# Optimization experiments

Hardware: AMD Instinct MI355X
Metric: run time of the kernel (lower is better)

Reference implementation:

```python
import jax, jax.numpy as jnp
import numpy as np

B, T, C_IN, H, W = 4, 128, 8, 32, 32
K = 9
HID = 64
N_BLOCKS = 2


def _conv(x, w, b):
    # x: [N, Cin, H, W], w: [Cout, Cin, 3, 3]
    y = jax.lax.conv_general_dilated(x, w, (1, 1), 'SAME',
                                     dimension_numbers=('NCHW', 'OIHW', 'NCHW'))
    return y + b[None, :, None, None]


def _refiner(x, w_in, b_in, w1s, b1s, w2s, b2s, w_out, b_out):
    # conv_in -> N_BLOCKS residual blocks -> conv_out (assumed LatentResidualRefiner structure)
    h = jax.nn.silu(_conv(x, w_in, b_in))
    for i in range(w1s.shape[0]):
        h = h + _conv(jax.nn.silu(_conv(h, w1s[i], b1s[i])), w2s[i], b2s[i])
    return _conv(h, w_out, b_out)


def setup_inputs() -> dict:
    key = jax.random.key(0)
    ks = jax.random.split(key, 8)
    latents = jax.random.normal(ks[0], (B, T, C_IN, H, W), dtype=jnp.float32)
    # distinct sorted anchor indices per batch row (duplicates would create zero-length gaps)
    idx = jax.vmap(lambda k: jnp.sort(jax.random.choice(k, T, (K,), replace=False)))(
        jax.random.split(ks[1], B)).astype(jnp.int32)
    in_ch = 3 * C_IN + 1   # z_base, z0, z1, t_chan (gap_cond=False)
    out_ch = C_IN + 1      # residual + uncertainty channel
    s = jnp.float32(0.05)
    w_in = jax.random.normal(ks[2], (HID, in_ch, 3, 3), jnp.float32) * s
    b_in = jnp.zeros((HID,), jnp.float32)
    w1s = jax.random.normal(ks[3], (N_BLOCKS, HID, HID, 3, 3), jnp.float32) * s
    b1s = jnp.zeros((N_BLOCKS, HID), jnp.float32)
    w2s = jax.random.normal(ks[4], (N_BLOCKS, HID, HID, 3, 3), jnp.float32) * s
    b2s = jnp.zeros((N_BLOCKS, HID), jnp.float32)
    w_out = jax.random.normal(ks[5], (out_ch, HID, 3, 3), jnp.float32) * s
    b_out = jnp.zeros((out_ch,), jnp.float32)
    return dict(latents=latents, idx=idx, w_in=w_in, b_in=b_in, w1s=w1s, b1s=b1s,
                w2s=w2s, b2s=b2s, w_out=w_out, b_out=b_out)


def reference(latents, idx, w_in, b_in, w1s, b1s, w2s, b2s, w_out, b_out):
    # Fully vectorized version of LatentLerpResidualInterpolator.interpolate:
    # every timestep finds its bracketing anchors (t0, t1); alpha clamping makes
    # anchors and out-of-range edges reduce exactly to the anchor latents
    # (scale = alpha*(1-alpha) = 0), matching the per-segment torch loop.
    Bb, Tt, C, Hh, Ww = latents.shape
    Kk = idx.shape[1]
    dt = latents.dtype
    idx_s = jnp.sort(idx, axis=1)                                   # [B,K]
    t = jnp.arange(Tt)
    seg = jax.vmap(lambda ib: jnp.searchsorted(ib, t, side='right'))(idx_s) - 1
    seg = jnp.clip(seg, 0, Kk - 2)                                  # [B,T]
    t0 = jnp.take_along_axis(idx_s, seg, axis=1)                    # [B,T]
    t1 = jnp.take_along_axis(idx_s, seg + 1, axis=1)                # [B,T]
    alpha_raw = (t[None, :] - t0).astype(dt) / jnp.maximum(t1 - t0, 1).astype(dt)
    alpha = jnp.clip(alpha_raw, 0.0, 1.0)                           # [B,T]
    gather = jax.vmap(lambda lat, i: lat[i])
    z0 = gather(latents, t0)                                        # [B,T,C,H,W]
    z1 = gather(latents, t1)
    a = alpha[:, :, None, None, None]
    z_base = (1.0 - a) * z0 + a * z1
    t_chan = jnp.broadcast_to(a, (Bb, Tt, 1, Hh, Ww)).astype(dt)
    res_in = jnp.concatenate([z_base, z0, z1, t_chan], axis=2)
    res_in = res_in.reshape(Bb * Tt, 3 * C + 1, Hh, Ww)
    out = _refiner(res_in, w_in, b_in, w1s, b1s, w2s, b2s, w_out, b_out)
    out = out.reshape(Bb, Tt, C + 1, Hh, Ww)
    res = out[:, :, :C]
    unc = jax.nn.sigmoid(out[:, :, C])                              # [B,T,H,W]
    z_hat = z_base + (a * (1.0 - a)) * res                          # [B,T,C,H,W]
    interior = (alpha_raw > 0.0) & (alpha_raw < 1.0)                # strict gap interior
    conf = jnp.where(interior[:, :, None, None],
                     jnp.clip(1.0 - unc, 0.0, 1.0), jnp.asarray(1.0, dt))
    return z_hat, conf
```

## Files before the change

kernel.cpp:

```cpp
#include <hip/hip_runtime.h>
#include <hip/hip_bf16.h>

#define DEVFN __device__ __forceinline__

typedef __attribute__((ext_vector_type(8))) short bf16x8;
typedef __attribute__((ext_vector_type(4))) float f32x4;

constexpr int T = 128, C = 8, K = 9;
constexpr int HW = 1024;
constexpr int BT = 512;
constexpr size_t Z_SIZE = (size_t)BT * C * HW;

constexpr int ROW_B = 34 * 128;
constexpr int BUF_B = 34 * ROW_B;

constexpr int WP_IN = 0;
constexpr int WP_W1_0 = 18432;
constexpr int WP_W2_0 = 55296;
constexpr int WP_W1_1 = 92160;
constexpr int WP_W2_1 = 129024;
constexpr int WP_OUT = 165888;
constexpr int WP_TOT = 175104;

DEVFN ushort f2bs(float x) {
  __hip_bfloat16 h = __float2bfloat16(x);
  ushort u;
  __builtin_memcpy(&u, &h, 2);
  return u;
}
DEVFN float bs2f(ushort u) {
  __hip_bfloat16 h;
  __builtin_memcpy(&h, &u, 2);
  return __bfloat162float(h);
}

DEVFN void interp_params(const int* __restrict__ idx, int b, int t,
                         int& t0, int& t1, float& ar, float& a) {
  const int* ib = idx + b * K;
  int cnt = 0;
#pragma unroll
  for (int k = 0; k < K; ++k) cnt += (ib[k] <= t) ? 1 : 0;
  int seg = min(max(cnt - 1, 0), K - 2);
  t0 = ib[seg];
  t1 = ib[seg + 1];
  ar = (float)(t - t0) / (float)max(t1 - t0, 1);
  a = fminf(fmaxf(ar, 0.f), 1.f);
}

__global__ __launch_bounds__(256) void pack_weights(
    const float* __restrict__ w_in, const float* __restrict__ w1s,
    const float* __restrict__ w2s, const float* __restrict__ w_out,
    __hip_bfloat16* __restrict__ wp) {
  int e = blockIdx.x * 256 + threadIdx.x;
  if (e >= WP_TOT) return;
  float v;
  if (e < WP_W1_0) {
    int tap = e / 2048;
    int r2 = e % 2048;
    int mt = r2 / 512;
    int lane = (r2 / 8) & 63;
    int el = e & 7;
    int oc = mt * 16 + (lane & 15);
    int ic = (lane >> 4) * 8 + el;
    v = (ic < 25) ? w_in[((size_t)oc * 25 + ic) * 9 + tap] : 0.f;
  } else if (e < WP_OUT) {
    int r = e - WP_W1_0;
    int layer = r / 36864;
    int r2 = r % 36864;
    int tap = r2 / 4096;
    int c = (r2 / 2048) & 1;
    int mt = (r2 / 512) & 3;
    int lane = (r2 / 8) & 63;
    int el = r2 & 7;
    int oc = mt * 16 + (lane & 15);
    int ic = c * 32 + (lane >> 4) * 8 + el;
    const float* src = (layer & 1) ? w2s : w1s;
    int blk = layer >> 1;
    v = src[(((size_t)blk * 64 + oc) * 64 + ic) * 9 + tap];
  } else {
    int r2 = e - WP_OUT;
    int tap = r2 / 1024;
    int c = (r2 / 512) & 1;
    int lane = (r2 / 8) & 63;
    int el = r2 & 7;
    int oc = lane & 15;
    int ic = c * 32 + (lane >> 4) * 8 + el;
    v = (oc < 9) ? w_out[((size_t)oc * 64 + ic) * 9 + tap] : 0.f;
  }
  wp[e] = __float2bfloat16(v);
}

template <int CK, int MT>
DEVFN void conv_compute(const char* sBuf, const __hip_bfloat16* __restrict__ wpf,
                        const int (&base)[3][2], int lane,
                        f32x4 (&acc)[MT][4]) {
#pragma unroll
  for (int c = 0; c < CK; ++c) {
#pragma unroll
    for (int d = 0; d < 3; ++d) {
      bf16x8 bv[4][2];
#pragma unroll
      for (int j = 0; j < 4; ++j)
#pragma unroll
        for (int xh = 0; xh < 2; ++xh)
          bv[j][xh] = *(const bf16x8*)(sBuf + base[d][c] + xh * 2048 + j * ROW_B);
#pragma unroll
      for (int mt = 0; mt < MT; ++mt) {
#pragma unroll
        for (int dyi = 0; dyi < 3; ++dyi) {
          const int tap = dyi * 3 + d;
          bf16x8 av =
              *(const bf16x8*)(wpf + (((tap * CK + c) * MT + mt) * 64 + lane) * 8);
#pragma unroll
          for (int oy = 0; oy < 2; ++oy)
#pragma unroll
            for (int xh = 0; xh < 2; ++xh)
              acc[mt][oy * 2 + xh] = __builtin_amdgcn_mfma_f32_16x16x32_bf16(
                  av, bv[oy + dyi][xh], acc[mt][oy * 2 + xh], 0, 0, 0);
        }
      }
    }
  }
}

DEVFN int wr_off(int nt) { return (nt & 1) * 2048 + ((nt >> 1) + 1) * ROW_B; }

DEVFN void layer_write_silu(char* sBuf, const int (&wbase)[4],
                            const float* __restrict__ bias, int g,
                            const f32x4 (&acc)[4][4]) {
#pragma unroll
  for (int mt = 0; mt < 4; ++mt) {
    const float4 bv = *(const float4*)(bias + mt * 16 + g * 4);
#pragma unroll
    for (int nt = 0; nt < 4; ++nt) {
      ushort4 s;
      float x0 = acc[mt][nt][0] + bv.x;
      float x1 = acc[mt][nt][1] + bv.y;
      float x2 = acc[mt][nt][2] + bv.z;
      float x3 = acc[mt][nt][3] + bv.w;
      s.x = f2bs(x0 / (1.f + expf(-x0)));
      s.y = f2bs(x1 / (1.f + expf(-x1)));
      s.z = f2bs(x2 / (1.f + expf(-x2)));
      s.w = f2bs(x3 / (1.f + expf(-x3)));
      *(ushort4*)(sBuf + wbase[mt] + wr_off(nt)) = s;
    }
  }
}

DEVFN void layer_write_bias(char* sBuf, const int (&wbase)[4],
                            const float* __restrict__ bias, int g,
                            const f32x4 (&acc)[4][4]) {
#pragma unroll
  for (int mt = 0; mt < 4; ++mt) {
    const float4 bv = *(const float4*)(bias + mt * 16 + g * 4);
#pragma unroll
    for (int nt = 0; nt < 4; ++nt) {
      ushort4 s;
      s.x = f2bs(acc[mt][nt][0] + bv.x);
      s.y = f2bs(acc[mt][nt][1] + bv.y);
      s.z = f2bs(acc[mt][nt][2] + bv.z);
      s.w = f2bs(acc[mt][nt][3] + bv.w);
      *(ushort4*)(sBuf + wbase[mt] + wr_off(nt)) = s;
    }
  }
}

__global__ __launch_bounds__(1024) void mega_kernel(
    const float* __restrict__ latents, const int* __restrict__ idx,
    const __hip_bfloat16* __restrict__ wpk, const float* __restrict__ b_in,
    const float* __restrict__ b1s, const float* __restrict__ b2s,
    const float* __restrict__ b_out, float* __restrict__ dout) {
  __shared__ __align__(16) char sBuf[BUF_B];

  const int img = blockIdx.x;
  const int tid = threadIdx.x;
  const int lane = tid & 63;
  const int wv = tid >> 6;
  const int g = lane >> 4;
  const int ln = lane & 15;
  const int r0 = wv * 2;
  const int b = img >> 7, t = img & 127;

  int t0, t1;
  float ar, a;
  interp_params(idx, b, t, t0, t1, ar, a);
  const float* z0p = latents + ((size_t)b * T + t0) * C * HW;
  const float* z1p = latents + ((size_t)b * T + t1) * C * HW;

  if (tid < 132) {
    int sy, sx;
    if (tid < 34) { sy = 0; sx = tid; }
    else if (tid < 68) { sy = 33; sx = tid - 34; }
    else { int r = tid - 68; sy = 1 + (r >> 1); sx = (r & 1) * 33; }
    int4* p4 = (int4*)(sBuf + sy * ROW_B + sx * 128);
#pragma unroll
    for (int q = 0; q < 8; ++q) p4[q] = int4{0, 0, 0, 0};
  }
  {
    const ushort ab = f2bs(a);
    const int si = tid;
    const int y = si >> 5, x = si & 31;
    const int sy = y + 1, sx = x + 1;
    const int key = (sx & 7) << 4;
    char* rowp = sBuf + sy * ROW_B + sx * 128;
    float v0[8], v1[8];
#pragma unroll
    for (int c2 = 0; c2 < 8; ++c2) {
      v0[c2] = z0p[c2 * HW + si];
      v1[c2] = z1p[c2 * HW + si];
    }
    ushort u[8];
    int4 q;
#pragma unroll
    for (int c2 = 0; c2 < 8; ++c2) u[c2] = f2bs((1.f - a) * v0[c2] + a * v1[c2]);
    q.x = (int)u[0] | ((int)u[1] << 16); q.y = (int)u[2] | ((int)u[3] << 16);
    q.z = (int)u[4] | ((int)u[5] << 16); q.w = (int)u[6] | ((int)u[7] << 16);
    *(int4*)(rowp + (0 ^ key)) = q;
#pragma unroll
    for (int c2 = 0; c2 < 8; ++c2) u[c2] = f2bs(v0[c2]);
    q.x = (int)u[0] | ((int)u[1] << 16); q.y = (int)u[2] | ((int)u[3] << 16);
    q.z = (int)u[4] | ((int)u[5] << 16); q.w = (int)u[6] | ((int)u[7] << 16);
    *(int4*)(rowp + (16 ^ key)) = q;
#pragma unroll
    for (int c2 = 0; c2 < 8; ++c2) u[c2] = f2bs(v1[c2]);
    q.x = (int)u[0] | ((int)u[1] << 16); q.y = (int)u[2] | ((int)u[3] << 16);
    q.z = (int)u[4] | ((int)u[5] << 16); q.w = (int)u[6] | ((int)u[7] << 16);
    *(int4*)(rowp + (32 ^ key)) = q;
    q.x = (int)ab; q.y = 0; q.z = 0; q.w = 0;
    *(int4*)(rowp + (48 ^ key)) = q;
  }
  __syncthreads();

  int base[3][2];
#pragma unroll
  for (int d = 0; d < 3; ++d)
#pragma unroll
    for (int c = 0; c < 2; ++c)
      base[d][c] = r0 * ROW_B +
                   (((ln + d) * 128 + c * 64 + g * 16) ^ (((ln + d) & 7) << 4));
  const int wkey = ((ln + 1) & 7) << 4;
  int wbase[4];
#pragma unroll
  for (int mt = 0; mt < 4; ++mt)
    wbase[mt] = r0 * ROW_B + (ln + 1) * 128 + ((mt * 32 + g * 8) ^ wkey);

  {
    f32x4 acc[4][4];
#pragma unroll
    for (int mt = 0; mt < 4; ++mt)
#pragma unroll
      for (int nt = 0; nt < 4; ++nt) acc[mt][nt] = (f32x4)0.f;
    conv_compute<1, 4>(sBuf, wpk + WP_IN, base, lane, acc);
    __syncthreads();
    layer_write_silu(sBuf, wbase, b_in, g, acc);
    __syncthreads();
  }

#pragma unroll 1
  for (int blk = 0; blk < 2; ++blk) {
    const __hip_bfloat16* wp1 = wpk + (blk ? WP_W1_1 : WP_W1_0);
    const __hip_bfloat16* wp2 = wpk + (blk ? WP_W2_1 : WP_W2_0);
    ushort4 hs[4][4];
    {
      f32x4 acc[4][4];
#pragma unroll
      for (int mt = 0; mt < 4; ++mt)
#pragma unroll
        for (int nt = 0; nt < 4; ++nt) acc[mt][nt] = (f32x4)0.f;
      conv_compute<2, 4>(sBuf, wp1, base, lane, acc);
#pragma unroll
      for (int mt = 0; mt < 4; ++mt)
#pragma unroll
        for (int nt = 0; nt < 4; ++nt)
          hs[mt][nt] = *(const ushort4*)(sBuf + wbase[mt] + wr_off(nt));
      __syncthreads();
      layer_write_silu(sBuf, wbase, b1s + blk * 64, g, acc);
      __syncthreads();
    }
    {
      f32x4 acc[4][4];
#pragma unroll
      for (int mt = 0; mt < 4; ++mt)
#pragma unroll
        for (int nt = 0; nt < 4; ++nt) {
          f32x4 h4;
          h4[0] = bs2f(hs[mt][nt].x);
          h4[1] = bs2f(hs[mt][nt].y);
          h4[2] = bs2f(hs[mt][nt].z);
          h4[3] = bs2f(hs[mt][nt].w);
          acc[mt][nt] = h4;
        }
      conv_compute<2, 4>(sBuf, wp2, base, lane, acc);
      __syncthreads();
      layer_write_bias(sBuf, wbase, b2s + blk * 64, g, acc);
      __syncthreads();
    }
  }

  {
    f32x4 acc[1][4];
#pragma unroll
    for (int nt = 0; nt < 4; ++nt) acc[0][nt] = (f32x4)0.f;
    conv_compute<2, 1>(sBuf, wpk + WP_OUT, base, lane, acc);
    __syncthreads();
#pragma unroll
    for (int nt = 0; nt < 4; ++nt) {
      ushort4 s;
      s.x = f2bs(acc[0][nt][0]);
      s.y = f2bs(acc[0][nt][1]);
      s.z = f2bs(acc[0][nt][2]);
      s.w = f2bs(acc[0][nt][3]);
      *(ushort4*)(sBuf + wbase[0] + wr_off(nt)) = s;
    }
    __syncthreads();
  }

  const bool interior = (ar > 0.f) && (ar < 1.f);
  const float aa = a * (1.f - a);
  {
    const int px = tid;
    const int y = px >> 5, x = px & 31;
    const int sy = y + 1, sx = x + 1;
    const int key = (sx & 7) << 4;
    const char* rp = sBuf + sy * ROW_B + sx * 128;
    bf16x8 r8 = *(const bf16x8*)(rp + (0 ^ key));
    int r9i = *(const int*)(rp + (16 ^ key));
    float res[9];
#pragma unroll
    for (int e = 0; e < 8; ++e) res[e] = bs2f((ushort)r8[e]);
    res[8] = bs2f((ushort)(r9i & 0xffff));
#pragma unroll
    for (int c2 = 0; c2 < 8; ++c2) {
      float v0 = z0p[c2 * HW + px], v1 = z1p[c2 * HW + px];
      float zb = (1.f - a) * v0 + a * v1;
      dout[((size_t)img * C + c2) * HW + px] = zb + aa * (res[c2] + b_out[c2]);
    }
    float unc = 1.f / (1.f + expf(-(res[8] + b_out[8])));
    float conf = interior ? fminf(fmaxf(1.f - unc, 0.f), 1.f) : 1.f;
    dout[Z_SIZE + (size_t)img * HW + px] = conf;
  }
}

extern "C" void kernel_launch(void* const* d_in, const int* in_sizes, int n_in,
                              void* d_out, int out_size, void* d_ws,
                              size_t ws_size, hipStream_t stream) {
  const float* latents = (const float*)d_in[0];
  const int* idx = (const int*)d_in[1];
  const float* w_in = (const float*)d_in[2];
  const float* b_in = (const float*)d_in[3];
  const float* w1s = (const float*)d_in[4];
  const float* b1s = (const float*)d_in[5];
  const float* w2s = (const float*)d_in[6];
  const float* b2s = (const float*)d_in[7];
  const float* w_out = (const float*)d_in[8];
  const float* b_out = (const float*)d_in[9];
  float* dout = (float*)d_out;

  __hip_bfloat16* wpk = (__hip_bfloat16*)d_ws;

  pack_weights<<<(WP_TOT + 255) / 256, 256, 0, stream>>>(w_in, w1s, w2s, w_out,
                                                         wpk);
  mega_kernel<<<BT, 1024, 0, stream>>>(latents, idx, wpk, b_in, b1s, b2s, b_out,
                                       dout);
}
```

Before: 283.4 us.

## Split fused per-image refiner into per-layer row-tiled conv kernels via global memory

Replaces the single 1024-thread-per-image megakernel with six launches, one per conv layer. Each launch uses 256-thread blocks that each handle an 8-row strip, and bf16 activations round-trip through workspace buffers in global memory, with the residual add done in the epilogue. The aim is smaller LDS footprint per block and a 4x larger grid for better occupancy and latency hiding. In exchange it adds global-memory traffic for intermediate activations (about 64 MB per layer), recomputes halo rows, and pays extra launch overhead.

```diff
diff --git a/kernel.cpp b/kernel.cpp
--- a/kernel.cpp
+++ b/kernel.cpp
@@ -11,8 +11,10 @@
 constexpr int BT = 512;
 constexpr size_t Z_SIZE = (size_t)BT * C * HW;
 
-constexpr int ROW_B = 34 * 128;
-constexpr int BUF_B = 34 * ROW_B;
+constexpr int SROW64 = 34 * 128;
+constexpr int TILE64 = 10 * SROW64;
+constexpr int SROW32 = 34 * 64;
+constexpr int TILE32 = 10 * SROW32;
 
 constexpr int WP_IN = 0;
 constexpr int WP_W1_0 = 18432;
@@ -90,10 +92,12 @@
   wp[e] = __float2bfloat16(v);
 }
 
-template <int CK, int MT>
+template <int CK, int MT, int SITE_B>
 DEVFN void conv_compute(const char* sBuf, const __hip_bfloat16* __restrict__ wpf,
-                        const int (&base)[3][2], int lane,
+                        const int (&base)[3][CK], int lane,
                         f32x4 (&acc)[MT][4]) {
+  constexpr int ROW = 34 * SITE_B;
+  constexpr int XH = 16 * SITE_B;
 #pragma unroll
   for (int c = 0; c < CK; ++c) {
 #pragma unroll
@@ -103,7 +107,7 @@
       for (int j = 0; j < 4; ++j)
 #pragma unroll
         for (int xh = 0; xh < 2; ++xh)
-          bv[j][xh] = *(const bf16x8*)(sBuf + base[d][c] + xh * 2048 + j * ROW_B);
+          bv[j][xh] = *(const bf16x8*)(sBuf + base[d][c] + xh * XH + j * ROW);
 #pragma unroll
       for (int mt = 0; mt < MT; ++mt) {
 #pragma unroll
@@ -123,62 +127,97 @@
   }
 }
 
-DEVFN int wr_off(int nt) { return (nt & 1) * 2048 + ((nt >> 1) + 1) * ROW_B; }
-
-DEVFN void layer_write_silu(char* sBuf, const int (&wbase)[4],
-                            const float* __restrict__ bias, int g,
-                            const f32x4 (&acc)[4][4]) {
+template <bool SILU, bool RESID>
+__global__ __launch_bounds__(256) void conv64_t(
+    const __hip_bfloat16* __restrict__ in,
+    const __hip_bfloat16* __restrict__ wpf,
+    const float* __restrict__ bias,
+    __hip_bfloat16* __restrict__ out) {
+  __shared__ __align__(16) char sBuf[TILE64];
+
+  const int img = blockIdx.x;
+  const int R0 = blockIdx.y * 8;
+  const int tid = threadIdx.x;
+  const int lane = tid & 63, wv = tid >> 6, g = lane >> 4, ln = lane & 15;
+  const int r0L = wv * 2;
+  const size_t imgBase = (size_t)img * HW * 64;
+
+  for (int e = tid; e < 2720; e += 256) {
+    int srow = e / 272;
+    int rem = e - srow * 272;
+    int sx = rem >> 3, slot = rem & 7;
+    int gy = R0 - 1 + srow, gx = sx - 1;
+    int4 v = int4{0, 0, 0, 0};
+    if (((unsigned)gy < 32u) & ((unsigned)gx < 32u))
+      v = *(const int4*)(in + imgBase + (size_t)(gy * 32 + gx) * 64 + slot * 8);
+    int dst = (srow * 34 + sx) * 128 + ((slot * 16) ^ ((sx & 7) << 4));
+    *(int4*)(sBuf + dst) = v;
+  }
+  __syncthreads();
+
+  int base[3][2];
+#pragma unroll
+  for (int d = 0; d < 3; ++d)
+#pragma unroll
+    for (int c = 0; c < 2; ++c)
+      base[d][c] = r0L * SROW64 +
+                   (((ln + d) * 128 + c * 64 + g * 16) ^ (((ln + d) & 7) << 4));
+
+  f32x4 acc[4][4];
+#pragma unroll
+  for (int mt = 0; mt < 4; ++mt)
+#pragma unroll
+    for (int nt = 0; nt < 4; ++nt) acc[mt][nt] = (f32x4)0.f;
+
+  conv_compute<2, 4, 128>(sBuf, wpf, base, lane, acc);
+
 #pragma unroll
   for (int mt = 0; mt < 4; ++mt) {
-    const float4 bv = *(const float4*)(bias + mt * 16 + g * 4);
+    const float4 bv4 = *(const float4*)(bias + mt * 16 + g * 4);
 #pragma unroll
     for (int nt = 0; nt < 4; ++nt) {
+      const int px = (R0 + r0L + (nt >> 1)) * 32 + (nt & 1) * 16 + ln;
+      __hip_bfloat16* op = (__hip_bfloat16*)(out + imgBase + (size_t)px * 64 +
+                                             mt * 16 + g * 4);
+      float v0 = acc[mt][nt][0] + bv4.x;
+      float v1 = acc[mt][nt][1] + bv4.y;
+      float v2 = acc[mt][nt][2] + bv4.z;
+      float v3 = acc[mt][nt][3] + bv4.w;
+      if (SILU) {
+        v0 = v0 / (1.f + expf(-v0));
+        v1 = v1 / (1.f + expf(-v1));
+        v2 = v2 / (1.f + expf(-v2));
+        v3 = v3 / (1.f + expf(-v3));
+      }
+      if (RESID) {
+        ushort4 h = *(const ushort4*)op;
+        v0 += bs2f(h.x);
+        v1 += bs2f(h.y);
+        v2 += bs2f(h.z);
+        v3 += bs2f(h.w);
+      }
       ushort4 s;
-      float x0 = acc[mt][nt][0] + bv.x;
-      float x1 = acc[mt][nt][1] + bv.y;
-      float x2 = acc[mt][nt][2] + bv.z;
-      float x3 = acc[mt][nt][3] + bv.w;
-      s.x = f2bs(x0 / (1.f + expf(-x0)));
-      s.y = f2bs(x1 / (1.f + expf(-x1)));
-      s.z = f2bs(x2 / (1.f + expf(-x2)));
-      s.w = f2bs(x3 / (1.f + expf(-x3)));
-      *(ushort4*)(sBuf + wbase[mt] + wr_off(nt)) = s;
+      s.x = f2bs(v0);
+      s.y = f2bs(v1);
+      s.z = f2bs(v2);
+      s.w = f2bs(v3);
+      *(ushort4*)op = s;
     }
   }
 }
 
-DEVFN void layer_write_bias(char* sBuf, const int (&wbase)[4],
-                            const float* __restrict__ bias, int g,
-                            const f32x4 (&acc)[4][4]) {
-#pragma unroll
-  for (int mt = 0; mt < 4; ++mt) {
-    const float4 bv = *(const float4*)(bias + mt * 16 + g * 4);
-#pragma unroll
-    for (int nt = 0; nt < 4; ++nt) {
-      ushort4 s;
-      s.x = f2bs(acc[mt][nt][0] + bv.x);
-      s.y = f2bs(acc[mt][nt][1] + bv.y);
-      s.z = f2bs(acc[mt][nt][2] + bv.z);
-      s.w = f2bs(acc[mt][nt][3] + bv.w);
-      *(ushort4*)(sBuf + wbase[mt] + wr_off(nt)) = s;
-    }
-  }
-}
-
-__global__ __launch_bounds__(1024) void mega_kernel(
+__global__ __launch_bounds__(256) void conv_in_t(
     const float* __restrict__ latents, const int* __restrict__ idx,
-    const __hip_bfloat16* __restrict__ wpk, const float* __restrict__ b_in,
-    const float* __restrict__ b1s, const float* __restrict__ b2s,
-    const float* __restrict__ b_out, float* __restrict__ dout) {
-  __shared__ __align__(16) char sBuf[BUF_B];
+    const __hip_bfloat16* __restrict__ wpf,
+    const float* __restrict__ bias,
+    __hip_bfloat16* __restrict__ out) {
+  __shared__ __align__(16) char sBuf[TILE32];
 
   const int img = blockIdx.x;
+  const int R0 = blockIdx.y * 8;
   const int tid = threadIdx.x;
-  const int lane = tid & 63;
-  const int wv = tid >> 6;
-  const int g = lane >> 4;
-  const int ln = lane & 15;
-  const int r0 = wv * 2;
+  const int lane = tid & 63, wv = tid >> 6, g = lane >> 4, ln = lane & 15;
+  const int r0L = wv * 2;
   const int b = img >> 7, t = img & 127;
 
   int t0, t1;
@@ -186,159 +225,157 @@
   interp_params(idx, b, t, t0, t1, ar, a);
   const float* z0p = latents + ((size_t)b * T + t0) * C * HW;
   const float* z1p = latents + ((size_t)b * T + t1) * C * HW;
-
-  if (tid < 132) {
-    int sy, sx;
-    if (tid < 34) { sy = 0; sx = tid; }
-    else if (tid < 68) { sy = 33; sx = tid - 34; }
-    else { int r = tid - 68; sy = 1 + (r >> 1); sx = (r & 1) * 33; }
-    int4* p4 = (int4*)(sBuf + sy * ROW_B + sx * 128);
-#pragma unroll
-    for (int q = 0; q < 8; ++q) p4[q] = int4{0, 0, 0, 0};
-  }
-  {
-    const ushort ab = f2bs(a);
-    const int si = tid;
-    const int y = si >> 5, x = si & 31;
-    const int sy = y + 1, sx = x + 1;
-    const int key = (sx & 7) << 4;
-    char* rowp = sBuf + sy * ROW_B + sx * 128;
-    float v0[8], v1[8];
-#pragma unroll
-    for (int c2 = 0; c2 < 8; ++c2) {
-      v0[c2] = z0p[c2 * HW + si];
-      v1[c2] = z1p[c2 * HW + si];
+  const ushort ab = f2bs(a);
+
+  for (int e = tid; e < 340; e += 256) {
+    int srow = e / 34, sx = e - srow * 34;
+    int gy = R0 - 1 + srow, gx = sx - 1;
+    char* sp = sBuf + srow * SROW32 + sx * 64;
+    const int key = (sx & 3) << 4;
+    if (((unsigned)gy < 32u) & ((unsigned)gx < 32u)) {
+      int p = gy * 32 + gx;
+      float v0[8], v1[8];
+#pragma unroll
+      for (int c2 = 0; c2 < 8; ++c2) {
+        v0[c2] = z0p[c2 * HW + p];
+        v1[c2] = z1p[c2 * HW + p];
+      }
+      ushort u[8];
+      int4 q;
+#pragma unroll
+      for (int c2 = 0; c2 < 8; ++c2) u[c2] = f2bs((1.f - a) * v0[c2] + a * v1[c2]);
+      q.x = (int)u[0] | ((int)u[1] << 16); q.y = (int)u[2] | ((int)u[3] << 16);
+      q.z = (int)u[4] | ((int)u[5] << 16); q.w = (int)u[6] | ((int)u[7] << 16);
+      *(int4*)(sp + (0 ^ key)) = q;
+#pragma unroll
+      for (int c2 = 0; c2 < 8; ++c2) u[c2] = f2bs(v0[c2]);
+      q.x = (int)u[0] | ((int)u[1] << 16); q.y = (int)u[2] | ((int)u[3] << 16);
+      q.z = (int)u[4] | ((int)u[5] << 16); q.w = (int)u[6] | ((int)u[7] << 16);
+      *(int4*)(sp + (16 ^ key)) = q;
+#pragma unroll
+      for (int c2 = 0; c2 < 8; ++c2) u[c2] = f2bs(v1[c2]);
+      q.x = (int)u[0] | ((int)u[1] << 16); q.y = (int)u[2] | ((int)u[3] << 16);
+      q.z = (int)u[4] | ((int)u[5] << 16); q.w = (int)u[6] | ((int)u[7] << 16);
+      *(int4*)(sp + (32 ^ key)) = q;
+      q.x = (int)ab; q.y = 0; q.z = 0; q.w = 0;
+      *(int4*)(sp + (48 ^ key)) = q;
+    } else {
+      int4 z = int4{0, 0, 0, 0};
+#pragma unroll
+      for (int s = 0; s < 4; ++s) *(int4*)(sp + ((s * 16) ^ key)) = z;
     }
-    ushort u[8];
-    int4 q;
-#pragma unroll
-    for (int c2 = 0; c2 < 8; ++c2) u[c2] = f2bs((1.f - a) * v0[c2] + a * v1[c2]);
-    q.x = (int)u[0] | ((int)u[1] << 16); q.y = (int)u[2] | ((int)u[3] << 16);
-    q.z = (int)u[4] | ((int)u[5] << 16); q.w = (int)u[6] | ((int)u[7] << 16);
-    *(int4*)(rowp + (0 ^ key)) = q;
-#pragma unroll
-    for (int c2 = 0; c2 < 8; ++c2) u[c2] = f2bs(v0[c2]);
-    q.x = (int)u[0] | ((int)u[1] << 16); q.y = (int)u[2] | ((int)u[3] << 16);
-    q.z = (int)u[4] | ((int)u[5] << 16); q.w = (int)u[6] | ((int)u[7] << 16);
-    *(int4*)(rowp + (16 ^ key)) = q;
-#pragma unroll
-    for (int c2 = 0; c2 < 8; ++c2) u[c2] = f2bs(v1[c2]);
-    q.x = (int)u[0] | ((int)u[1] << 16); q.y = (int)u[2] | ((int)u[3] << 16);
-    q.z = (int)u[4] | ((int)u[5] << 16); q.w = (int)u[6] | ((int)u[7] << 16);
-    *(int4*)(rowp + (32 ^ key)) = q;
-    q.x = (int)ab; q.y = 0; q.z = 0; q.w = 0;
-    *(int4*)(rowp + (48 ^ key)) = q;
   }
   __syncthreads();
 
+  int base[3][1];
+#pragma unroll
+  for (int d = 0; d < 3; ++d)
+    base[d][0] =
+        r0L * SROW32 + (((ln + d) * 64 + g * 16) ^ (((ln + d) & 3) << 4));
+
+  f32x4 acc[4][4];
+#pragma unroll
+  for (int mt = 0; mt < 4; ++mt)
+#pragma unroll
+    for (int nt = 0; nt < 4; ++nt) acc[mt][nt] = (f32x4)0.f;
+
+  conv_compute<1, 4, 64>(sBuf, wpf, base, lane, acc);
+
+  const size_t imgBase = (size_t)img * HW * 64;
+#pragma unroll
+  for (int mt = 0; mt < 4; ++mt) {
+    const float4 bv4 = *(const float4*)(bias + mt * 16 + g * 4);
+#pragma unroll
+    for (int nt = 0; nt < 4; ++nt) {
+      const int px = (R0 + r0L + (nt >> 1)) * 32 + (nt & 1) * 16 + ln;
+      float v0 = acc[mt][nt][0] + bv4.x;
+      float v1 = acc[mt][nt][1] + bv4.y;
+      float v2 = acc[mt][nt][2] + bv4.z;
+      float v3 = acc[mt][nt][3] + bv4.w;
+      ushort4 s;
+      s.x = f2bs(v0 / (1.f + expf(-v0)));
+      s.y = f2bs(v1 / (1.f + expf(-v1)));
+      s.z = f2bs(v2 / (1.f + expf(-v2)));
+      s.w = f2bs(v3 / (1.f + expf(-v3)));
+      *(ushort4*)(out + imgBase + (size_t)px * 64 + mt * 16 + g * 4) = s;
+    }
+  }
+}
+
+__global__ __launch_bounds__(256) void conv_final_t(
+    const __hip_bfloat16* __restrict__ in,
+    const __hip_bfloat16* __restrict__ wpf,
+    const float* __restrict__ bias,
+    const float* __restrict__ latents, const int* __restrict__ idx,
+    float* __restrict__ dout) {
+  __shared__ __align__(16) char sBuf[TILE64];
+  __shared__ float sOut[256][17];
+
+  const int img = blockIdx.x;
+  const int R0 = blockIdx.y * 8;
+  const int tid = threadIdx.x;
+  const int lane = tid & 63, wv = tid >> 6, g = lane >> 4, ln = lane & 15;
+  const int r0L = wv * 2;
+  const int b = img >> 7, t = img & 127;
+  const size_t imgBase = (size_t)img * HW * 64;
+
+  int t0, t1;
+  float ar, a;
+  interp_params(idx, b, t, t0, t1, ar, a);
+  const float* z0p = latents + ((size_t)b * T + t0) * C * HW;
+  const float* z1p = latents + ((size_t)b * T + t1) * C * HW;
+
+  for (int e = tid; e < 2720; e += 256) {
+    int srow = e / 272;
+    int rem = e - srow * 272;
+    int sx = rem >> 3, slot = rem & 7;
+    int gy = R0 - 1 + srow, gx = sx - 1;
+    int4 v = int4{0, 0, 0, 0};
+    if (((unsigned)gy < 32u) & ((unsigned)gx < 32u))
+      v = *(const int4*)(in + imgBase + (size_t)(gy * 32 + gx) * 64 + slot * 8);
+    int dst = (srow * 34 + sx) * 128 + ((slot * 16) ^ ((sx & 7) << 4));
+    *(int4*)(sBuf + dst) = v;
+  }
+  __syncthreads();
+
   int base[3][2];
 #pragma unroll
   for (int d = 0; d < 3; ++d)
 #pragma unroll
     for (int c = 0; c < 2; ++c)
-      base[d][c] = r0 * ROW_B +
+      base[d][c] = r0L * SROW64 +
                    (((ln + d) * 128 + c * 64 + g * 16) ^ (((ln + d) & 7) << 4));
-  const int wkey = ((ln + 1) & 7) << 4;
-  int wbase[4];
-#pragma unroll
-  for (int mt = 0; mt < 4; ++mt)
-    wbase[mt] = r0 * ROW_B + (ln + 1) * 128 + ((mt * 32 + g * 8) ^ wkey);
-
-  {
-    f32x4 acc[4][4];
-#pragma unroll
-    for (int mt = 0; mt < 4; ++mt)
-#pragma unroll
-      for (int nt = 0; nt < 4; ++nt) acc[mt][nt] = (f32x4)0.f;
-    conv_compute<1, 4>(sBuf, wpk + WP_IN, base, lane, acc);
-    __syncthreads();
-    layer_write_silu(sBuf, wbase, b_in, g, acc);
-    __syncthreads();
-  }
-
-#pragma unroll 1
-  for (int blk = 0; blk < 2; ++blk) {
-    const __hip_bfloat16* wp1 = wpk + (blk ? WP_W1_1 : WP_W1_0);
-    const __hip_bfloat16* wp2 = wpk + (blk ? WP_W2_1 : WP_W2_0);
-    ushort4 hs[4][4];
-    {
-      f32x4 acc[4][4];
-#pragma unroll
-      for (int mt = 0; mt < 4; ++mt)
-#pragma unroll
-        for (int nt = 0; nt < 4; ++nt) acc[mt][nt] = (f32x4)0.f;
-      conv_compute<2, 4>(sBuf, wp1, base, lane, acc);
-#pragma unroll
-      for (int mt = 0; mt < 4; ++mt)
-#pragma unroll
-        for (int nt = 0; nt < 4; ++nt)
-          hs[mt][nt] = *(const ushort4*)(sBuf + wbase[mt] + wr_off(nt));
-      __syncthreads();
-      layer_write_silu(sBuf, wbase, b1s + blk * 64, g, acc);
-      __syncthreads();
+
+  f32x4 acc[1][4];
+#pragma unroll
+  for (int nt = 0; nt < 4; ++nt) acc[0][nt] = (f32x4)0.f;
+
+  conv_compute<2, 1, 128>(sBuf, wpf, base, lane, acc);
+
+#pragma unroll
+  for (int nt = 0; nt < 4; ++nt) {
+    const int pxl = (r0L + (nt >> 1)) * 32 + (nt & 1) * 16 + ln;
+#pragma unroll
+    for (int r = 0; r < 4; ++r) {
+      const int oc = g * 4 + r;
+      sOut[pxl][oc] = acc[0][nt][r] + ((oc < 9) ? bias[oc] : 0.f);
     }
-    {
-      f32x4 acc[4][4];
-#pragma unroll
-      for (int mt = 0; mt < 4; ++mt)
-#pragma unroll
-        for (int nt = 0; nt < 4; ++nt) {
-          f32x4 h4;
-          h4[0] = bs2f(hs[mt][nt].x);
-          h4[1] = bs2f(hs[mt][nt].y);
-          h4[2] = bs2f(hs[mt][nt].z);
-          h4[3] = bs2f(hs[mt][nt].w);
-          acc[mt][nt] = h4;
-        }
-      conv_compute<2, 4>(sBuf, wp2, base, lane, acc);
-      __syncthreads();
-      layer_write_bias(sBuf, wbase, b2s + blk * 64, g, acc);
-      __syncthreads();
-    }
-  }
-
-  {
-    f32x4 acc[1][4];
-#pragma unroll
-    for (int nt = 0; nt < 4; ++nt) acc[0][nt] = (f32x4)0.f;
-    conv_compute<2, 1>(sBuf, wpk + WP_OUT, base, lane, acc);
-    __syncthreads();
-#pragma unroll
-    for (int nt = 0; nt < 4; ++nt) {
-      ushort4 s;
-      s.x = f2bs(acc[0][nt][0]);
-      s.y = f2bs(acc[0][nt][1]);
-      s.z = f2bs(acc[0][nt][2]);
-      s.w = f2bs(acc[0][nt][3]);
-      *(ushort4*)(sBuf + wbase[0] + wr_off(nt)) = s;
-    }
-    __syncthreads();
-  }
+  }
+  __syncthreads();
 
   const bool interior = (ar > 0.f) && (ar < 1.f);
   const float aa = a * (1.f - a);
-  {
-    const int px = tid;
-    const int y = px >> 5, x = px & 31;
-    const int sy = y + 1, sx = x + 1;
-    const int key = (sx & 7) << 4;
-    const char* rp = sBuf + sy * ROW_B + sx * 128;
-    bf16x8 r8 = *(const bf16x8*)(rp + (0 ^ key));
-    int r9i = *(const int*)(rp + (16 ^ key));
-    float res[9];
-#pragma unroll
-    for (int e = 0; e < 8; ++e) res[e] = bs2f((ushort)r8[e]);
-    res[8] = bs2f((ushort)(r9i & 0xffff));
-#pragma unroll
-    for (int c2 = 0; c2 < 8; ++c2) {
-      float v0 = z0p[c2 * HW + px], v1 = z1p[c2 * HW + px];
-      float zb = (1.f - a) * v0 + a * v1;
-      dout[((size_t)img * C + c2) * HW + px] = zb + aa * (res[c2] + b_out[c2]);
-    }
-    float unc = 1.f / (1.f + expf(-(res[8] + b_out[8])));
-    float conf = interior ? fminf(fmaxf(1.f - unc, 0.f), 1.f) : 1.f;
-    dout[Z_SIZE + (size_t)img * HW + px] = conf;
-  }
+  const int px = R0 * 32 + tid;
+#pragma unroll
+  for (int c2 = 0; c2 < 8; ++c2) {
+    float res = sOut[tid][c2];
+    float v0 = z0p[c2 * HW + px], v1 = z1p[c2 * HW + px];
+    float zb = (1.f - a) * v0 + a * v1;
+    dout[((size_t)img * C + c2) * HW + px] = zb + aa * res;
+  }
+  float unc = 1.f / (1.f + expf(-sOut[tid][8]));
+  float conf = interior ? fminf(fmaxf(1.f - unc, 0.f), 1.f) : 1.f;
+  dout[Z_SIZE + (size_t)img * HW + px] = conf;
 }
 
 extern "C" void kernel_launch(void* const* d_in, const int* in_sizes, int n_in,
@@ -356,10 +393,22 @@
   const float* b_out = (const float*)d_in[9];
   float* dout = (float*)d_out;
 
-  __hip_bfloat16* wpk = (__hip_bfloat16*)d_ws;
+  char* ws = (char*)d_ws;
+  __hip_bfloat16* A = (__hip_bfloat16*)ws;
+  __hip_bfloat16* Bb = (__hip_bfloat16*)(ws + (size_t)67108864);
+  __hip_bfloat16* wpk = (__hip_bfloat16*)(ws + (size_t)134217728);
 
   pack_weights<<<(WP_TOT + 255) / 256, 256, 0, stream>>>(w_in, w1s, w2s, w_out,
                                                          wpk);
-  mega_kernel<<<BT, 1024, 0, stream>>>(latents, idx, wpk, b_in, b1s, b2s, b_out,
-                                       dout);
-}
+
+  dim3 grid(BT, 4);
+  conv_in_t<<<grid, 256, 0, stream>>>(latents, idx, wpk + WP_IN, b_in, A);
+
+  conv64_t<true, false><<<grid, 256, 0, stream>>>(A, wpk + WP_W1_0, b1s, Bb);
+  conv64_t<false, true><<<grid, 256, 0, stream>>>(Bb, wpk + WP_W2_0, b2s, A);
+  conv64_t<true, false><<<grid, 256, 0, stream>>>(A, wpk + WP_W1_1, b1s + 64, Bb);
+  conv64_t<false, true><<<grid, 256, 0, stream>>>(Bb, wpk + WP_W2_1, b2s + 64, A);
+
+  conv_final_t<<<grid, 256, 0, stream>>>(A, wpk + WP_OUT, b_out, latents, idx,
+                                         dout);
+}
```

Measured after the change: 471.4 us. 1.66x slower.

## Shrink blocks to 256 threads with in-place row-pair conv and ring buffer

Applied to the files above, without the earlier changes.

Rewrites the fused refiner kernel to use 4 waves per image instead of 16. Each wave now walks four row-pairs per layer and writes its results back into one shared tile in place, using a small ring buffer and staggered writes so neighbouring rows are not overwritten before they are read. The residual stream is saved to a global workspace and reloaded, instead of being kept in LDS or registers. The goal is higher occupancy, since several blocks can share a CU, and each wave does more work per weight load. In exchange it adds global traffic for the residual, more barriers, and intricate ordering that could break correctness.

```diff
diff --git a/kernel.cpp b/kernel.cpp
--- a/kernel.cpp
+++ b/kernel.cpp
@@ -11,14 +11,10 @@
 constexpr int BT = 512;
 constexpr size_t Z_SIZE = (size_t)BT * C * HW;
 
-constexpr int ROW_B = 34 * 128;
-constexpr int BUF_B = 34 * ROW_B;
+constexpr int SR = 34 * 128;
 
 constexpr int WP_IN = 0;
 constexpr int WP_W1_0 = 18432;
-constexpr int WP_W2_0 = 55296;
-constexpr int WP_W1_1 = 92160;
-constexpr int WP_W2_1 = 129024;
 constexpr int WP_OUT = 165888;
 constexpr int WP_TOT = 175104;
 
@@ -90,12 +86,63 @@
   wp[e] = __float2bfloat16(v);
 }
 
-template <int CK, int MT>
-DEVFN void conv_compute(const char* sBuf, const __hip_bfloat16* __restrict__ wpf,
-                        const int (&base)[3][2], int lane,
-                        f32x4 (&acc)[MT][4]) {
-#pragma unroll
-  for (int c = 0; c < CK; ++c) {
+DEVFN void pack_held(const f32x4 (&acc)[4][4], const float* __restrict__ bias,
+                     bool silu, int g, ushort4 (&held)[16]) {
+#pragma unroll
+  for (int mt = 0; mt < 4; ++mt) {
+    const float4 b4 = *(const float4*)(bias + mt * 16 + g * 4);
+#pragma unroll
+    for (int nt = 0; nt < 4; ++nt) {
+      float v0 = acc[mt][nt][0] + b4.x;
+      float v1 = acc[mt][nt][1] + b4.y;
+      float v2 = acc[mt][nt][2] + b4.z;
+      float v3 = acc[mt][nt][3] + b4.w;
+      if (silu) {
+        v0 = v0 / (1.f + expf(-v0));
+        v1 = v1 / (1.f + expf(-v1));
+        v2 = v2 / (1.f + expf(-v2));
+        v3 = v3 / (1.f + expf(-v3));
+      }
+      ushort4 s;
+      s.x = f2bs(v0);
+      s.y = f2bs(v1);
+      s.z = f2bs(v2);
+      s.w = f2bs(v3);
+      held[mt * 4 + nt] = s;
+    }
+  }
+}
+
+template <int CK>
+DEVFN void compute_pair(const char* tile, const int (&rb)[3][2],
+                        const __hip_bfloat16* __restrict__ wpf,
+                        const __hip_bfloat16* hg, bool resid, int p, int lane,
+                        int g, int ln, f32x4 (&acc)[4][4]) {
+  if (resid) {
+#pragma unroll
+    for (int mt = 0; mt < 4; ++mt)
+#pragma unroll
+      for (int oy = 0; oy < 2; ++oy)
+#pragma unroll
+        for (int xh = 0; xh < 2; ++xh) {
+          const int px = (2 * p + oy) * 32 + xh * 16 + ln;
+          ushort4 h4 = *(const ushort4*)(hg + (size_t)px * 64 + mt * 16 + g * 4);
+          f32x4 a4;
+          a4[0] = bs2f(h4.x);
+          a4[1] = bs2f(h4.y);
+          a4[2] = bs2f(h4.z);
+          a4[3] = bs2f(h4.w);
+          acc[mt][oy * 2 + xh] = a4;
+        }
+  } else {
+#pragma unroll
+    for (int mt = 0; mt < 4; ++mt)
+#pragma unroll
+      for (int nt = 0; nt < 4; ++nt) acc[mt][nt] = (f32x4)0.f;
+  }
+  const int rowOff = 2 * p * SR;
+#pragma unroll
+  for (int c = 0; c < CK; ++c)
 #pragma unroll
     for (int d = 0; d < 3; ++d) {
       bf16x8 bv[4][2];
@@ -103,14 +150,17 @@
       for (int j = 0; j < 4; ++j)
 #pragma unroll
         for (int xh = 0; xh < 2; ++xh)
-          bv[j][xh] = *(const bf16x8*)(sBuf + base[d][c] + xh * 2048 + j * ROW_B);
-#pragma unroll
-      for (int mt = 0; mt < MT; ++mt) {
+          bv[j][xh] = *(const bf16x8*)(tile + rowOff + j * SR + rb[d][c] +
+                                       xh * 2048);
+#pragma unroll
+      for (int mt = 0; mt < 4; ++mt)
 #pragma unroll
         for (int dyi = 0; dyi < 3; ++dyi) {
-          const int tap = dyi * 3 + d;
-          bf16x8 av =
-              *(const bf16x8*)(wpf + (((tap * CK + c) * MT + mt) * 64 + lane) * 8);
+          bf16x8 av = *(const bf16x8*)(wpf +
+                                       ((((dyi * 3 + d) * CK + c) * 4 + mt) *
+                                            64 +
+                                        lane) *
+                                           8);
 #pragma unroll
           for (int oy = 0; oy < 2; ++oy)
 #pragma unroll
@@ -118,67 +168,141 @@
               acc[mt][oy * 2 + xh] = __builtin_amdgcn_mfma_f32_16x16x32_bf16(
                   av, bv[oy + dyi][xh], acc[mt][oy * 2 + xh], 0, 0, 0);
         }
-      }
-    }
-  }
-}
-
-DEVFN int wr_off(int nt) { return (nt & 1) * 2048 + ((nt >> 1) + 1) * ROW_B; }
-
-DEVFN void layer_write_silu(char* sBuf, const int (&wbase)[4],
-                            const float* __restrict__ bias, int g,
-                            const f32x4 (&acc)[4][4]) {
-#pragma unroll
-  for (int mt = 0; mt < 4; ++mt) {
-    const float4 bv = *(const float4*)(bias + mt * 16 + g * 4);
-#pragma unroll
-    for (int nt = 0; nt < 4; ++nt) {
-      ushort4 s;
-      float x0 = acc[mt][nt][0] + bv.x;
-      float x1 = acc[mt][nt][1] + bv.y;
-      float x2 = acc[mt][nt][2] + bv.z;
-      float x3 = acc[mt][nt][3] + bv.w;
-      s.x = f2bs(x0 / (1.f + expf(-x0)));
-      s.y = f2bs(x1 / (1.f + expf(-x1)));
-      s.z = f2bs(x2 / (1.f + expf(-x2)));
-      s.w = f2bs(x3 / (1.f + expf(-x3)));
-      *(ushort4*)(sBuf + wbase[mt] + wr_off(nt)) = s;
-    }
-  }
-}
-
-DEVFN void layer_write_bias(char* sBuf, const int (&wbase)[4],
-                            const float* __restrict__ bias, int g,
-                            const f32x4 (&acc)[4][4]) {
-#pragma unroll
-  for (int mt = 0; mt < 4; ++mt) {
-    const float4 bv = *(const float4*)(bias + mt * 16 + g * 4);
-#pragma unroll
-    for (int nt = 0; nt < 4; ++nt) {
-      ushort4 s;
-      s.x = f2bs(acc[mt][nt][0] + bv.x);
-      s.y = f2bs(acc[mt][nt][1] + bv.y);
-      s.z = f2bs(acc[mt][nt][2] + bv.z);
-      s.w = f2bs(acc[mt][nt][3] + bv.w);
-      *(ushort4*)(sBuf + wbase[mt] + wr_off(nt)) = s;
-    }
-  }
-}
-
-__global__ __launch_bounds__(1024) void mega_kernel(
+    }
+}
+
+DEVFN void write_tile(char* tile, const ushort4 (&held)[16], int p, int g,
+                      int ln) {
+#pragma unroll
+  for (int mt = 0; mt < 4; ++mt)
+#pragma unroll
+    for (int oy = 0; oy < 2; ++oy)
+#pragma unroll
+      for (int xh = 0; xh < 2; ++xh) {
+        const int sx = 1 + xh * 16 + ln;
+        const int addr = (2 * p + 1 + oy) * SR + sx * 128 +
+                         ((mt * 32 + g * 8) ^ ((sx & 7) << 4));
+        *(ushort4*)(tile + addr) = held[mt * 4 + oy * 2 + xh];
+      }
+}
+
+DEVFN void write_ring(char* ring, const ushort4 (&held)[16], int g, int ln) {
+#pragma unroll
+  for (int mt = 0; mt < 4; ++mt)
+#pragma unroll
+    for (int oy = 0; oy < 2; ++oy)
+#pragma unroll
+      for (int xh = 0; xh < 2; ++xh) {
+        const int sxr = xh * 16 + ln;
+        const int addr =
+            oy * 4096 + sxr * 128 + ((mt * 32 + g * 8) ^ ((sxr & 7) << 4));
+        *(ushort4*)(ring + addr) = held[mt * 4 + oy * 2 + xh];
+      }
+}
+
+DEVFN void ring_to_tile(char* tile, const char* ring, int p, int lane) {
+  const int rowr = lane >> 5, pxr = lane & 31;
+  const int key_r = (pxr & 7) << 4;
+  const int key_t = (((pxr + 1) & 7) << 4);
+  const char* rp = ring + rowr * 4096 + pxr * 128;
+  char* tp = tile + (2 * p + 1 + rowr) * SR + (pxr + 1) * 128;
+#pragma unroll
+  for (int q = 0; q < 8; ++q) {
+    int4 v = *(const int4*)(rp + ((q * 16) ^ key_r));
+    *(int4*)(tp + ((q * 16) ^ key_t)) = v;
+  }
+}
+
+DEVFN void store_h(__hip_bfloat16* hg, const ushort4 (&held)[16], int p, int g,
+                   int ln) {
+#pragma unroll
+  for (int mt = 0; mt < 4; ++mt)
+#pragma unroll
+    for (int oy = 0; oy < 2; ++oy)
+#pragma unroll
+      for (int xh = 0; xh < 2; ++xh) {
+        const int px = (2 * p + oy) * 32 + xh * 16 + ln;
+        *(ushort4*)(hg + (size_t)px * 64 + mt * 16 + g * 4) =
+            held[mt * 4 + oy * 2 + xh];
+      }
+}
+
+template <int CK>
+DEVFN void run_layer(char* tile, char* ring, const int (&rb)[3][2],
+                     const __hip_bfloat16* __restrict__ wpf,
+                     const float* __restrict__ bias, __hip_bfloat16* hg,
+                     bool silu, bool resid, bool storeh, int wv, int lane,
+                     int g, int ln) {
+  ushort4 h0[16];
+  f32x4 acc[4][4];
+  const bool w3 = (wv == 3);
+
+  compute_pair<CK>(tile, rb, wpf, hg, resid, wv, lane, g, ln, acc);
+  pack_held(acc, bias, silu, g, h0);
+  if (storeh) store_h(hg, h0, wv, g, ln);
+  __syncthreads();
+
+  if (!w3) write_tile(tile, h0, wv, g, ln);
+  compute_pair<CK>(tile, rb, wpf, hg, resid, 4 + wv, lane, g, ln, acc);
+  {
+    ushort4 cur[16];
+    pack_held(acc, bias, silu, g, cur);
+    if (storeh) store_h(hg, cur, 4 + wv, g, ln);
+    if (!w3) {
+#pragma unroll
+      for (int i = 0; i < 16; ++i) h0[i] = cur[i];
+    } else {
+      write_ring(ring, cur, g, ln);
+    }
+  }
+  __syncthreads();
+
+  write_tile(tile, h0, w3 ? 3 : 4 + wv, g, ln);
+  compute_pair<CK>(tile, rb, wpf, hg, resid, 8 + wv, lane, g, ln, acc);
+  pack_held(acc, bias, silu, g, h0);
+  if (storeh) store_h(hg, h0, 8 + wv, g, ln);
+  __syncthreads();
+
+  if (!w3) {
+    write_tile(tile, h0, 8 + wv, g, ln);
+  } else {
+    ring_to_tile(tile, ring, 7, lane);
+  }
+  compute_pair<CK>(tile, rb, wpf, hg, resid, 12 + wv, lane, g, ln, acc);
+  {
+    ushort4 cur[16];
+    pack_held(acc, bias, silu, g, cur);
+    if (storeh) store_h(hg, cur, 12 + wv, g, ln);
+    if (!w3) {
+#pragma unroll
+      for (int i = 0; i < 16; ++i) h0[i] = cur[i];
+    } else {
+      write_ring(ring, cur, g, ln);
+    }
+  }
+  __syncthreads();
+
+  if (!w3) {
+    write_tile(tile, h0, 12 + wv, g, ln);
+  } else {
+    write_tile(tile, h0, 11, g, ln);
+    ring_to_tile(tile, ring, 15, lane);
+  }
+  __syncthreads();
+}
+
+__global__ __launch_bounds__(256) void mega256(
     const float* __restrict__ latents, const int* __restrict__ idx,
     const __hip_bfloat16* __restrict__ wpk, const float* __restrict__ b_in,
     const float* __restrict__ b1s, const float* __restrict__ b2s,
-    const float* __restrict__ b_out, float* __restrict__ dout) {
-  __shared__ __align__(16) char sBuf[BUF_B];
+    const float* __restrict__ b_out, __hip_bfloat16* hglob,
+    float* __restrict__ dout) {
+  __shared__ __align__(16) char tile[34 * SR];
+  __shared__ __align__(16) char ring[8192];
 
   const int img = blockIdx.x;
   const int tid = threadIdx.x;
-  const int lane = tid & 63;
-  const int wv = tid >> 6;
-  const int g = lane >> 4;
-  const int ln = lane & 15;
-  const int r0 = wv * 2;
+  const int lane = tid & 63, wv = tid >> 6, g = lane >> 4, ln = lane & 15;
   const int b = img >> 7, t = img & 127;
 
   int t0, t1;
@@ -186,158 +310,152 @@
   interp_params(idx, b, t, t0, t1, ar, a);
   const float* z0p = latents + ((size_t)b * T + t0) * C * HW;
   const float* z1p = latents + ((size_t)b * T + t1) * C * HW;
+  __hip_bfloat16* hg = hglob + (size_t)img * HW * 64;
 
   if (tid < 132) {
     int sy, sx;
-    if (tid < 34) { sy = 0; sx = tid; }
-    else if (tid < 68) { sy = 33; sx = tid - 34; }
-    else { int r = tid - 68; sy = 1 + (r >> 1); sx = (r & 1) * 33; }
-    int4* p4 = (int4*)(sBuf + sy * ROW_B + sx * 128);
+    if (tid < 34) {
+      sy = 0;
+      sx = tid;
+    } else if (tid < 68) {
+      sy = 33;
+      sx = tid - 34;
+    } else {
+      int r = tid - 68;
+      sy = 1 + (r >> 1);
+      sx = (r & 1) * 33;
+    }
+    int4* p4 = (int4*)(tile + sy * SR + sx * 128);
 #pragma unroll
     for (int q = 0; q < 8; ++q) p4[q] = int4{0, 0, 0, 0};
   }
   {
     const ushort ab = f2bs(a);
-    const int si = tid;
-    const int y = si >> 5, x = si & 31;
-    const int sy = y + 1, sx = x + 1;
-    const int key = (sx & 7) << 4;
-    char* rowp = sBuf + sy * ROW_B + sx * 128;
-    float v0[8], v1[8];
-#pragma unroll
-    for (int c2 = 0; c2 < 8; ++c2) {
-      v0[c2] = z0p[c2 * HW + si];
-      v1[c2] = z1p[c2 * HW + si];
-    }
-    ushort u[8];
-    int4 q;
-#pragma unroll
-    for (int c2 = 0; c2 < 8; ++c2) u[c2] = f2bs((1.f - a) * v0[c2] + a * v1[c2]);
-    q.x = (int)u[0] | ((int)u[1] << 16); q.y = (int)u[2] | ((int)u[3] << 16);
-    q.z = (int)u[4] | ((int)u[5] << 16); q.w = (int)u[6] | ((int)u[7] << 16);
-    *(int4*)(rowp + (0 ^ key)) = q;
-#pragma unroll
-    for (int c2 = 0; c2 < 8; ++c2) u[c2] = f2bs(v0[c2]);
-    q.x = (int)u[0] | ((int)u[1] << 16); q.y = (int)u[2] | ((int)u[3] << 16);
-    q.z = (int)u[4] | ((int)u[5] << 16); q.w = (int)u[6] | ((int)u[7] << 16);
-    *(int4*)(rowp + (16 ^ key)) = q;
-#pragma unroll
-    for (int c2 = 0; c2 < 8; ++c2) u[c2] = f2bs(v1[c2]);
-    q.x = (int)u[0] | ((int)u[1] << 16); q.y = (int)u[2] | ((int)u[3] << 16);
-    q.z = (int)u[4] | ((int)u[5] << 16); q.w = (int)u[6] | ((int)u[7] << 16);
-    *(int4*)(rowp + (32 ^ key)) = q;
-    q.x = (int)ab; q.y = 0; q.z = 0; q.w = 0;
-    *(int4*)(rowp + (48 ^ key)) = q;
-  }
-  __syncthreads();
-
-  int base[3][2];
+#pragma unroll
+    for (int k2 = 0; k2 < 4; ++k2) {
+      const int si = tid + k2 * 256;
+      const int y = si >> 5, x = si & 31;
+      char* sp = tile + (y + 1) * SR + (x + 1) * 128;
+      const int key = ((x + 1) & 7) << 4;
+      float v0[8], v1[8];
+#pragma unroll
+      for (int c2 = 0; c2 < 8; ++c2) {
+        v0[c2] = z0p[c2 * HW + si];
+        v1[c2] = z1p[c2 * HW + si];
+      }
+      ushort u[8];
+      int4 q;
+#pragma unroll
+      for (int c2 = 0; c2 < 8; ++c2)
+        u[c2] = f2bs((1.f - a) * v0[c2] + a * v1[c2]);
+      q.x = (int)u[0] | ((int)u[1] << 16);
+      q.y = (int)u[2] | ((int)u[3] << 16);
+      q.z = (int)u[4] | ((int)u[5] << 16);
+      q.w = (int)u[6] | ((int)u[7] << 16);
+      *(int4*)(sp + (0 ^ key)) = q;
+#pragma unroll
+      for (int c2 = 0; c2 < 8; ++c2) u[c2] = f2bs(v0[c2]);
+      q.x = (int)u[0] | ((int)u[1] << 16);
+      q.y = (int)u[2] | ((int)u[3] << 16);
+      q.z = (int)u[4] | ((int)u[5] << 16);
+      q.w = (int)u[6] | ((int)u[7] << 16);
+      *(int4*)(sp + (16 ^ key)) = q;
+#pragma unroll
+      for (int c2 = 0; c2 < 8; ++c2) u[c2] = f2bs(v1[c2]);
+      q.x = (int)u[0] | ((int)u[1] << 16);
+      q.y = (int)u[2] | ((int)u[3] << 16);
+      q.z = (int)u[4] | ((int)u[5] << 16);
+      q.w = (int)u[6] | ((int)u[7] << 16);
+      *(int4*)(sp + (32 ^ key)) = q;
+      q.x = (int)ab;
+      q.y = 0;
+      q.z = 0;
+      q.w = 0;
+      *(int4*)(sp + (48 ^ key)) = q;
+    }
+  }
+  __syncthreads();
+
+  int rb[3][2];
 #pragma unroll
   for (int d = 0; d < 3; ++d)
 #pragma unroll
     for (int c = 0; c < 2; ++c)
-      base[d][c] = r0 * ROW_B +
-                   (((ln + d) * 128 + c * 64 + g * 16) ^ (((ln + d) & 7) << 4));
-  const int wkey = ((ln + 1) & 7) << 4;
-  int wbase[4];
-#pragma unroll
-  for (int mt = 0; mt < 4; ++mt)
-    wbase[mt] = r0 * ROW_B + (ln + 1) * 128 + ((mt * 32 + g * 8) ^ wkey);
-
-  {
-    f32x4 acc[4][4];
-#pragma unroll
-    for (int mt = 0; mt < 4; ++mt)
-#pragma unroll
-      for (int nt = 0; nt < 4; ++nt) acc[mt][nt] = (f32x4)0.f;
-    conv_compute<1, 4>(sBuf, wpk + WP_IN, base, lane, acc);
-    __syncthreads();
-    layer_write_silu(sBuf, wbase, b_in, g, acc);
-    __syncthreads();
-  }
+      rb[d][c] =
+          (((ln + d) * 128 + c * 64 + g * 16) ^ (((ln + d) & 7) << 4));
+
+  run_layer<1>(tile, ring, rb, wpk + WP_IN, b_in, hg, true, false, true, wv,
+               lane, g, ln);
 
 #pragma unroll 1
   for (int blk = 0; blk < 2; ++blk) {
-    const __hip_bfloat16* wp1 = wpk + (blk ? WP_W1_1 : WP_W1_0);
-    const __hip_bfloat16* wp2 = wpk + (blk ? WP_W2_1 : WP_W2_0);
-    ushort4 hs[4][4];
-    {
-      f32x4 acc[4][4];
-#pragma unroll
-      for (int mt = 0; mt < 4; ++mt)
-#pragma unroll
-        for (int nt = 0; nt < 4; ++nt) acc[mt][nt] = (f32x4)0.f;
-      conv_compute<2, 4>(sBuf, wp1, base, lane, acc);
-#pragma unroll
-      for (int mt = 0; mt < 4; ++mt)
-#pragma unroll
-        for (int nt = 0; nt < 4; ++nt)
-          hs[mt][nt] = *(const ushort4*)(sBuf + wbase[mt] + wr_off(nt));
-      __syncthreads();
-      layer_write_silu(sBuf, wbase, b1s + blk * 64, g, acc);
-      __syncthreads();
-    }
-    {
-      f32x4 acc[4][4];
-#pragma unroll
-      for (int mt = 0; mt < 4; ++mt)
-#pragma unroll
-        for (int nt = 0; nt < 4; ++nt) {
-          f32x4 h4;
-          h4[0] = bs2f(hs[mt][nt].x);
-          h4[1] = bs2f(hs[mt][nt].y);
-          h4[2] = bs2f(hs[mt][nt].z);
-          h4[3] = bs2f(hs[mt][nt].w);
-          acc[mt][nt] = h4;
-        }
-      conv_compute<2, 4>(sBuf, wp2, base, lane, acc);
-      __syncthreads();
-      layer_write_bias(sBuf, wbase, b2s + blk * 64, g, acc);
-      __syncthreads();
-    }
-  }
-
-  {
-    f32x4 acc[1][4];
-#pragma unroll
-    for (int nt = 0; nt < 4; ++nt) acc[0][nt] = (f32x4)0.f;
-    conv_compute<2, 1>(sBuf, wpk + WP_OUT, base, lane, acc);
-    __syncthreads();
-#pragma unroll
-    for (int nt = 0; nt < 4; ++nt) {
-      ushort4 s;
-      s.x = f2bs(acc[0][nt][0]);
-      s.y = f2bs(acc[0][nt][1]);
-      s.z = f2bs(acc[0][nt][2]);
-      s.w = f2bs(acc[0][nt][3]);
-      *(ushort4*)(sBuf + wbase[0] + wr_off(nt)) = s;
-    }
-    __syncthreads();
+#pragma unroll 1
+    for (int cc = 0; cc < 2; ++cc) {
+      const __hip_bfloat16* wp = wpk + WP_W1_0 + (blk * 2 + cc) * 36864;
+      const float* bias = cc ? (b2s + blk * 64) : (b1s + blk * 64);
+      const bool silu = (cc == 0);
+      const bool resid = (cc == 1);
+      const bool storeh = (cc == 1) && (blk == 0);
+      run_layer<2>(tile, ring, rb, wp, bias, hg, silu, resid, storeh, wv, lane,
+                   g, ln);
+    }
   }
 
   const bool interior = (ar > 0.f) && (ar < 1.f);
   const float aa = a * (1.f - a);
-  {
-    const int px = tid;
-    const int y = px >> 5, x = px & 31;
-    const int sy = y + 1, sx = x + 1;
-    const int key = (sx & 7) << 4;
-    const char* rp = sBuf + sy * ROW_B + sx * 128;
-    bf16x8 r8 = *(const bf16x8*)(rp + (0 ^ key));
-    int r9i = *(const int*)(rp + (16 ^ key));
-    float res[9];
-#pragma unroll
-    for (int e = 0; e < 8; ++e) res[e] = bs2f((ushort)r8[e]);
-    res[8] = bs2f((ushort)(r9i & 0xffff));
-#pragma unroll
-    for (int c2 = 0; c2 < 8; ++c2) {
-      float v0 = z0p[c2 * HW + px], v1 = z1p[c2 * HW + px];
-      float zb = (1.f - a) * v0 + a * v1;
-      dout[((size_t)img * C + c2) * HW + px] = zb + aa * (res[c2] + b_out[c2]);
-    }
-    float unc = 1.f / (1.f + expf(-(res[8] + b_out[8])));
-    float conf = interior ? fminf(fmaxf(1.f - unc, 0.f), 1.f) : 1.f;
-    dout[Z_SIZE + (size_t)img * HW + px] = conf;
+  const __hip_bfloat16* wpO = wpk + WP_OUT;
+#pragma unroll 1
+  for (int s = 0; s < 4; ++s) {
+    const int p = 4 * s + wv;
+    f32x4 facc[4];
+#pragma unroll
+    for (int nt = 0; nt < 4; ++nt) facc[nt] = (f32x4)0.f;
+    const int rowOff = 2 * p * SR;
+#pragma unroll
+    for (int c = 0; c < 2; ++c)
+#pragma unroll
+      for (int d = 0; d < 3; ++d) {
+        bf16x8 bv[4][2];
+#pragma unroll
+        for (int j = 0; j < 4; ++j)
+#pragma unroll
+          for (int xh = 0; xh < 2; ++xh)
+            bv[j][xh] = *(const bf16x8*)(tile + rowOff + j * SR + rb[d][c] +
+                                         xh * 2048);
+#pragma unroll
+        for (int dyi = 0; dyi < 3; ++dyi) {
+          bf16x8 av = *(const bf16x8*)(wpO +
+                                       (((dyi * 3 + d) * 2 + c) * 64 + lane) *
+                                           8);
+#pragma unroll
+          for (int oy = 0; oy < 2; ++oy)
+#pragma unroll
+            for (int xh = 0; xh < 2; ++xh)
+              facc[oy * 2 + xh] = __builtin_amdgcn_mfma_f32_16x16x32_bf16(
+                  av, bv[oy + dyi][xh], facc[oy * 2 + xh], 0, 0, 0);
+        }
+      }
+#pragma unroll
+    for (int oy = 0; oy < 2; ++oy)
+#pragma unroll
+      for (int xh = 0; xh < 2; ++xh) {
+        const int nt = oy * 2 + xh;
+        const int px = (2 * p + oy) * 32 + xh * 16 + ln;
+        if (g < 2) {
+#pragma unroll
+          for (int r = 0; r < 4; ++r) {
+            const int c2 = g * 4 + r;
+            float res = facc[nt][r] + b_out[c2];
+            float v0 = z0p[c2 * HW + px], v1 = z1p[c2 * HW + px];
+            float zb = (1.f - a) * v0 + a * v1;
+            dout[((size_t)img * C + c2) * HW + px] = zb + aa * res;
+          }
+        } else if (g == 2) {
+          float unc = 1.f / (1.f + expf(-(facc[nt][0] + b_out[8])));
+          float conf = interior ? fminf(fmaxf(1.f - unc, 0.f), 1.f) : 1.f;
+          dout[Z_SIZE + (size_t)img * HW + px] = conf;
+        }
+      }
   }
 }
 
@@ -356,10 +474,12 @@
   const float* b_out = (const float*)d_in[9];
   float* dout = (float*)d_out;
 
-  __hip_bfloat16* wpk = (__hip_bfloat16*)d_ws;
+  char* ws = (char*)d_ws;
+  __hip_bfloat16* hglob = (__hip_bfloat16*)ws;
+  __hip_bfloat16* wpk = (__hip_bfloat16*)(ws + (size_t)67108864);
 
   pack_weights<<<(WP_TOT + 255) / 256, 256, 0, stream>>>(w_in, w1s, w2s, w_out,
                                                          wpk);
-  mega_kernel<<<BT, 1024, 0, stream>>>(latents, idx, wpk, b_in, b1s, b2s, b_out,
-                                       dout);
-}
+  mega256<<<BT, 256, 0, stream>>>(latents, idx, wpk, b_in, b1s, b2s, b_out,
+                                  hglob, dout);
+}
```

Result: slower. 514.9 us (+81.7%).
